# Performance work log

Measured on AMD Instinct MI355X. Metric: run time of the kernel, lower is better.

The kernel has to match this reference:

```python
import jax, jax.numpy as jnp
import numpy as np
from jax import lax

# Model hyperparameters (from module source: D_state=2, Expand=1; mamba-ssm defaults)
B_, C_, H_, W_ = 16, 128, 96, 96
D_MODEL = C_
D_INNER = 1 * D_MODEL          # expand = 1
D_STATE = 2
DT_RANK = (D_MODEL + 15) // 16  # ceil(d_model/16) = 8
D_CONV = 4
OUT_C = 128
LN_EPS = 1e-5


def setup_inputs() -> dict:
    key = jax.random.key(0)
    ks = jax.random.split(key, 10)
    s = 0.02
    x = jax.random.normal(ks[0], (B_, C_, H_, W_), dtype=jnp.float32)
    in_proj_w = jax.random.normal(ks[1], (2 * D_INNER, D_MODEL), dtype=jnp.float32) * s
    conv_w = jax.random.normal(ks[2], (D_INNER, 1, D_CONV), dtype=jnp.float32) * s
    conv_b = jnp.zeros((D_INNER,), dtype=jnp.float32)
    x_proj_w = jax.random.normal(ks[3], (DT_RANK + 2 * D_STATE, D_INNER), dtype=jnp.float32) * s
    dt_proj_w = jax.random.normal(ks[4], (D_INNER, DT_RANK), dtype=jnp.float32) * s
    # softplus^{-1}(0.01) so initial dt ~ 0.01 (standard mamba init)
    dt_proj_b = jnp.full((D_INNER,), float(np.log(np.expm1(0.01))), dtype=jnp.float32)
    A_log = jnp.log(jnp.broadcast_to(jnp.arange(1, D_STATE + 1, dtype=jnp.float32), (D_INNER, D_STATE)))
    D_param = jnp.ones((D_INNER,), dtype=jnp.float32)
    out_proj_w = jax.random.normal(ks[5], (OUT_C, D_INNER), dtype=jnp.float32) * s
    ln_gamma = jnp.ones((OUT_C,), dtype=jnp.float32)
    ln_beta = jnp.zeros((OUT_C,), dtype=jnp.float32)
    return {
        "x": x, "in_proj_w": in_proj_w, "conv_w": conv_w, "conv_b": conv_b,
        "x_proj_w": x_proj_w, "dt_proj_w": dt_proj_w, "dt_proj_b": dt_proj_b,
        "A_log": A_log, "D_param": D_param, "out_proj_w": out_proj_w,
        "ln_gamma": ln_gamma, "ln_beta": ln_beta,
    }


def _ssm_cha(x, in_proj_w, conv_w, conv_b, x_proj_w, dt_proj_w, dt_proj_b,
             A_log, D_param, out_proj_w, ln_gamma, ln_beta):
    b, c, h, w = x.shape
    L = h * w
    tokens = x.transpose(0, 2, 3, 1).reshape(b, L, c)  # [b, L, d_model]

    # in_proj -> (x_in, z)
    xz = jnp.einsum("bld,ed->ble", tokens, in_proj_w)  # [b, L, 2*d_inner]
    x_in, z = jnp.split(xz, 2, axis=-1)

    # causal depthwise conv1d over L, then SiLU
    xc = x_in.transpose(0, 2, 1)  # [b, d_inner, L]
    xc = lax.conv_general_dilated(
        xc, conv_w, window_strides=(1,), padding=[(D_CONV - 1, 0)],
        dimension_numbers=("NCH", "OIH", "NCH"), feature_group_count=D_INNER,
    ) + conv_b[None, :, None]
    x_in = jax.nn.silu(xc).transpose(0, 2, 1)  # [b, L, d_inner]

    # x_proj -> (dt, B, C)
    x_dbl = jnp.einsum("bld,ed->ble", x_in, x_proj_w)
    dt = x_dbl[..., :DT_RANK]
    Bc = x_dbl[..., DT_RANK:DT_RANK + D_STATE]         # [b, L, n]
    Cc = x_dbl[..., DT_RANK + D_STATE:]                # [b, L, n]
    dt = jax.nn.softplus(jnp.einsum("blr,dr->bld", dt, dt_proj_w) + dt_proj_b)

    # selective scan (diagonal A) via associative scan over L
    A = -jnp.exp(A_log)                                # [d_inner, n]
    dA = jnp.exp(dt[..., None] * A)                    # [b, L, d_inner, n]
    dBx = dt[..., None] * Bc[:, :, None, :] * x_in[..., None]

    def combine(e1, e2):
        a1, b1 = e1
        a2, b2 = e2
        return a1 * a2, a2 * b1 + b2

    _, hstate = lax.associative_scan(combine, (dA, dBx), axis=1)  # [b, L, d, n]
    y = jnp.sum(hstate * Cc[:, :, None, :], axis=-1) + D_param * x_in  # [b, L, d]

    y = y * jax.nn.silu(z)
    out = jnp.einsum("bld,od->blo", y, out_proj_w)     # [b, L, out_c]

    # LayerNorm over out_c
    mu = jnp.mean(out, axis=-1, keepdims=True)
    var = jnp.mean(jnp.square(out - mu), axis=-1, keepdims=True)
    out = (out - mu) * lax.rsqrt(var + LN_EPS) * ln_gamma + ln_beta

    return out.reshape(b, h, w, OUT_C).transpose(0, 3, 1, 2)


def reference(x, in_proj_w, conv_w, conv_b, x_proj_w, dt_proj_w, dt_proj_b,
              A_log, D_param, out_proj_w, ln_gamma, ln_beta):
    return _ssm_cha(x, in_proj_w, conv_w, conv_b, x_proj_w, dt_proj_w, dt_proj_b,
                    A_log, D_param, out_proj_w, ln_gamma, ln_beta)
```

## Files before the change

### kernel.cpp

```cpp
#include <hip/hip_runtime.h>
#include <hip/hip_bf16.h>

#define B_N 16
#define L_N 9216
#define LT64 144

typedef __attribute__((ext_vector_type(8))) short short8;
typedef __attribute__((ext_vector_type(4))) float floatx4;

__device__ __forceinline__ float bfu(unsigned short u) {
  return __uint_as_float(((unsigned int)u) << 16);
}
__device__ __forceinline__ unsigned short fbf(float f) {
  __hip_bfloat16 h = __float2bfloat16(f);
  return *(unsigned short*)&h;
}

__global__ __launch_bounds__(256) void k_prep(const float* __restrict__ w1,
                                              const float* __restrict__ w2,
                                              __hip_bfloat16* __restrict__ w1bt,
                                              __hip_bfloat16* __restrict__ w2bt) {
  int i = blockIdx.x * 256 + threadIdx.x;
  if (i < 256 * 128) w1bt[i] = __float2bfloat16(w1[i]);
  if (i < 128 * 128) w2bt[i] = __float2bfloat16(w2[i]);
}

__global__ __launch_bounds__(256) void k_inproj_conv(
    const float* __restrict__ x, const __hip_bfloat16* __restrict__ w1bt,
    const float* __restrict__ cw, const float* __restrict__ cb,
    const float* __restrict__ xpw,
    __hip_bfloat16* __restrict__ xinb, __hip_bfloat16* __restrict__ zb,
    float* __restrict__ xdblT) {
  __shared__ __align__(16) char smem1[16384];
  __shared__ __align__(16) char smem2[34816];
  __hip_bfloat16* xs = (__hip_bfloat16*)smem1;
  float (*red)[12][64] = (float(*)[12][64])smem1;
  unsigned short (*st)[73] = (unsigned short(*)[73])smem2;
  float (*cvs)[68] = (float(*)[68])smem2;

  int blk = blockIdx.x, b = blk / LT64, lt = blk % LT64, l0 = lt * 64;
  int t = threadIdx.x;

  const float* xb = x + (size_t)b * 128 * L_N + (l0 - 8);
#pragma unroll
  for (int i = 0; i < 9; ++i) {
    int idx = t + i * 256;
    int c = idx / 18, q = idx % 18;
    float4 v;
    if (lt == 0 && q < 2) { v.x = 0.f; v.y = 0.f; v.z = 0.f; v.w = 0.f; }
    else v = *(const float4*)(xb + (size_t)c * L_N + q * 4);
    st[c][q * 4 + 0] = fbf(v.x); st[c][q * 4 + 1] = fbf(v.y);
    st[c][q * 4 + 2] = fbf(v.z); st[c][q * 4 + 3] = fbf(v.w);
  }

  int lane = t & 63, wv = t >> 6;
  int col = lane & 15, quad = lane >> 4;
  int e0 = wv * 64;
  short8 afr[4][4];
  const __hip_bfloat16* wb = w1bt + (size_t)(e0 + col) * 128 + quad * 8;
#pragma unroll
  for (int mi = 0; mi < 4; ++mi)
#pragma unroll
    for (int ks = 0; ks < 4; ++ks)
      afr[mi][ks] = *(const short8*)(wb + mi * 16 * 128 + ks * 32);

  __syncthreads();

#pragma unroll
  for (int p = 0; p < 4; ++p) {
    int gi = t + p * 256;
    int l = gi >> 4, ch = gi & 15;
    short8 cc;
#pragma unroll
    for (int j = 0; j < 8; ++j) cc[j] = (short)st[ch * 8 + j][8 + l];
    *(short8*)&xs[l * 128 + ((ch ^ (l & 7)) * 8)] = cc;
  }

  floatx4 vzero = {0.f, 0.f, 0.f, 0.f};
  floatx4 acc[4][4];
#pragma unroll
  for (int mi = 0; mi < 4; ++mi)
#pragma unroll
    for (int ni = 0; ni < 4; ++ni) acc[mi][ni] = vzero;
  __syncthreads();

#pragma unroll
  for (int ks = 0; ks < 4; ++ks) {
    short8 bfr[4];
#pragma unroll
    for (int ni = 0; ni < 4; ++ni) {
      int row = ni * 16 + col;
      bfr[ni] = *(const short8*)&xs[row * 128 + (((ks * 4 + quad) ^ (row & 7)) * 8)];
    }
#pragma unroll
    for (int mi = 0; mi < 4; ++mi)
#pragma unroll
      for (int ni = 0; ni < 4; ++ni)
        acc[mi][ni] = __builtin_amdgcn_mfma_f32_16x16x32_bf16(afr[mi][ks], bfr[ni], acc[mi][ni], 0, 0, 0);
  }

  float s0 = 0.f, s1 = 0.f, s2 = 0.f;
  if (t < 128 && lt > 0) {
    const __hip_bfloat16* wr = w1bt + (size_t)t * 128;
#pragma unroll
    for (int c8 = 0; c8 < 16; ++c8) {
      short8 wc = *(const short8*)(wr + c8 * 8);
#pragma unroll
      for (int e = 0; e < 8; ++e) {
        int c = c8 * 8 + e;
        float wf = bfu((unsigned short)wc[e]);
        s0 += wf * bfu(st[c][5]);
        s1 += wf * bfu(st[c][6]);
        s2 += wf * bfu(st[c][7]);
      }
    }
  }
  if (wv >= 2) {
    __hip_bfloat16* zbase = zb + ((size_t)b * 128 + (e0 - 128)) * L_N + l0;
#pragma unroll
    for (int mi = 0; mi < 4; ++mi)
#pragma unroll
      for (int r = 0; r < 4; ++r) {
        int dr = mi * 16 + quad * 4 + r;
#pragma unroll
        for (int ni = 0; ni < 4; ++ni)
          zbase[(size_t)dr * L_N + ni * 16 + col] = __float2bfloat16(acc[mi][ni][r]);
      }
  }
  __syncthreads();

  if (t < 128) { cvs[t][0] = s0; cvs[t][1] = s1; cvs[t][2] = s2; }
  if (wv < 2) {
#pragma unroll
    for (int mi = 0; mi < 4; ++mi)
#pragma unroll
      for (int r = 0; r < 4; ++r) {
        int d = e0 + mi * 16 + quad * 4 + r;
#pragma unroll
        for (int ni = 0; ni < 4; ++ni) cvs[d][3 + ni * 16 + col] = acc[mi][ni][r];
      }
  }
  __syncthreads();

  float part[12];
#pragma unroll
  for (int m = 0; m < 12; ++m) part[m] = 0.f;
  for (int dd = 0; dd < 32; ++dd) {
    int d = wv * 32 + dd;
    float v = cb[d] + cw[d * 4 + 0] * cvs[d][lane] + cw[d * 4 + 1] * cvs[d][lane + 1]
                    + cw[d * 4 + 2] * cvs[d][lane + 2] + cw[d * 4 + 3] * cvs[d][lane + 3];
    v = v / (1.f + __expf(-v));
    xinb[((size_t)b * 128 + d) * L_N + l0 + lane] = __float2bfloat16(v);
#pragma unroll
    for (int m = 0; m < 12; ++m) part[m] += xpw[m * 128 + d] * v;
  }
#pragma unroll
  for (int m = 0; m < 12; ++m) red[wv][m][lane] = part[m];
  __syncthreads();
  for (int idx = t; idx < 12 * 64; idx += 256) {
    int m = idx >> 6, l = idx & 63;
    float s = red[0][m][l] + red[1][m][l] + red[2][m][l] + red[3][m][l];
    xdblT[((size_t)b * 12 + m) * L_N + l0 + l] = s;
  }
}

__global__ __launch_bounds__(256) void k_scan(
    const float* __restrict__ xdblT, const float* __restrict__ dtw,
    const float* __restrict__ dtb, const float* __restrict__ alog,
    const float* __restrict__ dpar,
    const __hip_bfloat16* __restrict__ xinb, const __hip_bfloat16* __restrict__ zb,
    __hip_bfloat16* __restrict__ yb) {
  __shared__ float agg[4][4];
  __shared__ float carry[2];
  int blk = blockIdx.x, b = blk >> 7, d = blk & 127;
  int t = threadIdx.x, lane = t & 63, wv = t >> 6;
  float A0 = -__expf(alog[2 * d]), A1 = -__expf(alog[2 * d + 1]);
  float Dv = dpar[d], dtbv = dtb[d];
  float w[8];
#pragma unroll
  for (int i = 0; i < 8; ++i) w[i] = dtw[d * 8 + i];
  if (t == 0) { carry[0] = 0.f; carry[1] = 0.f; }
  __syncthreads();
  const float* xdT = xdblT + (size_t)b * 12 * L_N;
  const unsigned short* xi = (const unsigned short*)xinb + ((size_t)b * 128 + d) * L_N;
  const unsigned short* zr = (const unsigned short*)zb + ((size_t)b * 128 + d) * L_N;
  unsigned short* yo = (unsigned short*)yb + ((size_t)b * 128 + d) * L_N;
  for (int it = 0; it < 9; ++it) {
    int lb = it * 1024 + t * 4;
    float4 q[12];
#pragma unroll
    for (int m = 0; m < 12; ++m) q[m] = *(const float4*)(xdT + (size_t)m * L_N + lb);
    ushort4 xu = *(const ushort4*)(xi + lb);
    ushort4 zu = *(const ushort4*)(zr + lb);
    float xv[4] = {bfu(xu.x), bfu(xu.y), bfu(xu.z), bfu(xu.w)};
    float zv[4] = {bfu(zu.x), bfu(zu.y), bfu(zu.z), bfu(zu.w)};
    float A0p[4], X0p[4], A1p[4], X1p[4];
#pragma unroll
    for (int j = 0; j < 4; ++j) {
      float dtp = dtbv;
#pragma unroll
      for (int m = 0; m < 8; ++m) dtp += w[m] * ((const float*)&q[m])[j];
      float dt = (dtp > 15.f) ? dtp : __logf(1.f + __expf(dtp));
      float a0 = __expf(dt * A0), a1 = __expf(dt * A1);
      float dtx = dt * xv[j];
      float x0 = dtx * ((const float*)&q[8])[j];
      float x1 = dtx * ((const float*)&q[9])[j];
      if (j == 0) { A0p[0] = a0; X0p[0] = x0; A1p[0] = a1; X1p[0] = x1; }
      else {
        A0p[j] = a0 * A0p[j - 1]; X0p[j] = a0 * X0p[j - 1] + x0;
        A1p[j] = a1 * A1p[j - 1]; X1p[j] = a1 * X1p[j - 1] + x1;
      }
    }
    float wA0 = A0p[3], wX0 = X0p[3], wA1 = A1p[3], wX1 = X1p[3];
#pragma unroll
    for (int off = 1; off < 64; off <<= 1) {
      float pA0 = __shfl_up(wA0, off, 64), pX0 = __shfl_up(wX0, off, 64);
      float pA1 = __shfl_up(wA1, off, 64), pX1 = __shfl_up(wX1, off, 64);
      if (lane >= off) {
        wX0 += wA0 * pX0; wA0 *= pA0;
        wX1 += wA1 * pX1; wA1 *= pA1;
      }
    }
    if (lane == 63) { agg[wv][0] = wA0; agg[wv][1] = wX0; agg[wv][2] = wA1; agg[wv][3] = wX1; }
    float eA0 = __shfl_up(wA0, 1, 64), eX0 = __shfl_up(wX0, 1, 64);
    float eA1 = __shfl_up(wA1, 1, 64), eX1 = __shfl_up(wX1, 1, 64);
    if (lane == 0) { eA0 = 1.f; eX0 = 0.f; eA1 = 1.f; eX1 = 0.f; }
    __syncthreads();
    float h0 = carry[0], h1 = carry[1];
    for (int jw = 0; jw < wv; ++jw) {
      h0 = agg[jw][0] * h0 + agg[jw][1];
      h1 = agg[jw][2] * h1 + agg[jw][3];
    }
    h0 = eA0 * h0 + eX0;
    h1 = eA1 * h1 + eX1;
    __syncthreads();
    if (t == 255) { carry[0] = A0p[3] * h0 + X0p[3]; carry[1] = A1p[3] * h1 + X1p[3]; }
    ushort4 yu;
    unsigned short* yp = (unsigned short*)&yu;
#pragma unroll
    for (int j = 0; j < 4; ++j) {
      float hh0 = A0p[j] * h0 + X0p[j];
      float hh1 = A1p[j] * h1 + X1p[j];
      float y = hh0 * ((const float*)&q[10])[j] + hh1 * ((const float*)&q[11])[j] + Dv * xv[j];
      y *= zv[j] / (1.f + __expf(-zv[j]));
      yp[j] = fbf(y);
    }
    *(ushort4*)(yo + lb) = yu;
  }
}

__global__ __launch_bounds__(256) void k_outln(
    const __hip_bfloat16* __restrict__ yb, const __hip_bfloat16* __restrict__ w2bt,
    const float* __restrict__ gam, const float* __restrict__ bet,
    float* __restrict__ out) {
  __shared__ unsigned short st[128][68];
  __shared__ __hip_bfloat16 yts[64 * 128];
  __shared__ float red_s[4][64], red_q[4][64];
  __shared__ float gs[128], bs[128];
  int blk = blockIdx.x, b = blk / LT64, lt = blk % LT64, l0 = lt * 64;
  int t = threadIdx.x;
  if (t < 128) { gs[t] = gam[t]; bs[t] = bet[t]; }
  const unsigned short* ybb = (const unsigned short*)yb + (size_t)b * 128 * L_N + l0;
#pragma unroll
  for (int i = 0; i < 8; ++i) {
    int idx = t + i * 256;
    int dd = idx >> 4, l4 = (idx & 15) * 4;
    ushort4 v = *(const ushort4*)(ybb + (size_t)dd * L_N + l4);
    *(ushort4*)&st[dd][l4] = v;
  }
  __syncthreads();
#pragma unroll
  for (int p = 0; p < 4; ++p) {
    int gi = t + p * 256;
    int l = gi & 63, ch = gi >> 6;
    short8 c;
#pragma unroll
    for (int j = 0; j < 8; ++j) c[j] = (short)st[ch * 8 + j][l];
    *(short8*)&yts[l * 128 + ((ch ^ (l & 7)) * 8)] = c;
  }
  int lane = t & 63, wv = t >> 6;
  int col = lane & 15, quad = lane >> 4;
  int o0 = wv * 32;
  short8 afr[2][4];
#pragma unroll
  for (int mi = 0; mi < 2; ++mi)
#pragma unroll
    for (int ks = 0; ks < 4; ++ks)
      afr[mi][ks] = *(const short8*)(w2bt + (size_t)(o0 + mi * 16 + col) * 128 + ks * 32 + quad * 8);
  floatx4 vzero = {0.f, 0.f, 0.f, 0.f};
  floatx4 acc[2][4];
#pragma unroll
  for (int mi = 0; mi < 2; ++mi)
#pragma unroll
    for (int ni = 0; ni < 4; ++ni) acc[mi][ni] = vzero;
  __syncthreads();
#pragma unroll
  for (int ks = 0; ks < 4; ++ks) {
    short8 bfr[4];
#pragma unroll
    for (int ni = 0; ni < 4; ++ni) {
      int row = ni * 16 + col;
      bfr[ni] = *(const short8*)&yts[row * 128 + (((ks * 4 + quad) ^ (row & 7)) * 8)];
    }
#pragma unroll
    for (int mi = 0; mi < 2; ++mi)
#pragma unroll
      for (int ni = 0; ni < 4; ++ni)
        acc[mi][ni] = __builtin_amdgcn_mfma_f32_16x16x32_bf16(afr[mi][ks], bfr[ni], acc[mi][ni], 0, 0, 0);
  }
  float s[4], q[4];
#pragma unroll
  for (int ni = 0; ni < 4; ++ni) {
    float ss = 0.f, qq = 0.f;
#pragma unroll
    for (int mi = 0; mi < 2; ++mi)
#pragma unroll
      for (int r = 0; r < 4; ++r) {
        float v = acc[mi][ni][r];
        ss += v; qq += v * v;
      }
    ss += __shfl_xor(ss, 16, 64); ss += __shfl_xor(ss, 32, 64);
    qq += __shfl_xor(qq, 16, 64); qq += __shfl_xor(qq, 32, 64);
    s[ni] = ss; q[ni] = qq;
  }
  if (quad == 0) {
#pragma unroll
    for (int ni = 0; ni < 4; ++ni) {
      red_s[wv][ni * 16 + col] = s[ni];
      red_q[wv][ni * 16 + col] = q[ni];
    }
  }
  __syncthreads();
  float mu[4], rstd[4];
#pragma unroll
  for (int ni = 0; ni < 4; ++ni) {
    int li = ni * 16 + col;
    float ts = red_s[0][li] + red_s[1][li] + red_s[2][li] + red_s[3][li];
    float tq = red_q[0][li] + red_q[1][li] + red_q[2][li] + red_q[3][li];
    float m = ts * (1.f / 128.f);
    float var = tq * (1.f / 128.f) - m * m;
    mu[ni] = m;
    rstd[ni] = rsqrtf(var + 1e-5f);
  }
  float* ob = out + (size_t)b * 128 * L_N;
#pragma unroll
  for (int mi = 0; mi < 2; ++mi)
#pragma unroll
    for (int r = 0; r < 4; ++r) {
      int o = o0 + mi * 16 + quad * 4 + r;
      float g = gs[o], bb = bs[o];
#pragma unroll
      for (int ni = 0; ni < 4; ++ni)
        ob[(size_t)o * L_N + l0 + ni * 16 + col] = (acc[mi][ni][r] - mu[ni]) * rstd[ni] * g + bb;
    }
}

extern "C" void kernel_launch(void* const* d_in, const int* in_sizes, int n_in,
                              void* d_out, int out_size, void* d_ws, size_t ws_size,
                              hipStream_t stream) {
  const float* x    = (const float*)d_in[0];
  const float* w1   = (const float*)d_in[1];
  const float* cw   = (const float*)d_in[2];
  const float* cb   = (const float*)d_in[3];
  const float* xpw  = (const float*)d_in[4];
  const float* dtw  = (const float*)d_in[5];
  const float* dtb  = (const float*)d_in[6];
  const float* alog = (const float*)d_in[7];
  const float* dpar = (const float*)d_in[8];
  const float* w2   = (const float*)d_in[9];
  const float* gam  = (const float*)d_in[10];
  const float* bet  = (const float*)d_in[11];
  float* out = (float*)d_out;

  float* ws = (float*)d_ws;
  const size_t NBL = (size_t)B_N * 128 * L_N;
  float* xdblT = ws;
  __hip_bfloat16* xinb = (__hip_bfloat16*)(ws + (size_t)B_N * 12 * L_N);
  __hip_bfloat16* zb   = xinb + NBL;
  __hip_bfloat16* yb   = zb + NBL;
  __hip_bfloat16* w1bt = yb + NBL;
  __hip_bfloat16* w2bt = w1bt + 256 * 128;

  k_prep<<<128, 256, 0, stream>>>(w1, w2, w1bt, w2bt);
  k_inproj_conv<<<B_N * LT64, 256, 0, stream>>>(x, w1bt, cw, cb, xpw, xinb, zb, xdblT);
  k_scan<<<B_N * 128, 256, 0, stream>>>(xdblT, dtw, dtb, alog, dpar, xinb, zb, yb);
  k_outln<<<B_N * LT64, 256, 0, stream>>>(yb, w2bt, gam, bet, out);
}
```

Baseline: 321.6 us.

## Halve in-proj/conv shared memory by direct swizzled staging and two-pass conv

The x tile is now converted and written straight into the swizzled bf16 GEMM operand layout, with only the 3-column causal halo kept in a small separate buffer. This removes the intermediate transposed staging array and its extra barrier and transpose pass. The conv/SiLU/x_proj stage is split into two 64-channel passes so the conv buffer holds half the channels, roughly halving LDS per block to allow more resident blocks. The cost is an extra pair of barriers and scattered 2-byte LDS writes with possible bank conflicts during staging.

```diff
diff --git a/kernel.cpp b/kernel.cpp
--- a/kernel.cpp
+++ b/kernel.cpp
@@ -32,49 +32,46 @@
     __hip_bfloat16* __restrict__ xinb, __hip_bfloat16* __restrict__ zb,
     float* __restrict__ xdblT) {
   __shared__ __align__(16) char smem1[16384];
-  __shared__ __align__(16) char smem2[34816];
-  __hip_bfloat16* xs = (__hip_bfloat16*)smem1;
+  __shared__ __align__(16) char smem2[17408];
+  unsigned short* xs = (unsigned short*)smem1;
   float (*red)[12][64] = (float(*)[12][64])smem1;
-  unsigned short (*st)[73] = (unsigned short(*)[73])smem2;
+  unsigned short (*halo)[128] = (unsigned short(*)[128])smem2;
   float (*cvs)[68] = (float(*)[68])smem2;
 
   int blk = blockIdx.x, b = blk / LT64, lt = blk % LT64, l0 = lt * 64;
   int t = threadIdx.x;
+  int lane = t & 63, wv = t >> 6;
+  int col = lane & 15, quad = lane >> 4;
+  int e0 = wv * 64;
 
   const float* xb = x + (size_t)b * 128 * L_N + (l0 - 8);
 #pragma unroll
   for (int i = 0; i < 9; ++i) {
     int idx = t + i * 256;
-    int c = idx / 18, q = idx % 18;
+    int c = idx & 127, q = idx >> 7;
+    if (q == 0) continue;
     float4 v;
     if (lt == 0 && q < 2) { v.x = 0.f; v.y = 0.f; v.z = 0.f; v.w = 0.f; }
     else v = *(const float4*)(xb + (size_t)c * L_N + q * 4);
-    st[c][q * 4 + 0] = fbf(v.x); st[c][q * 4 + 1] = fbf(v.y);
-    st[c][q * 4 + 2] = fbf(v.z); st[c][q * 4 + 3] = fbf(v.w);
-  }
-
-  int lane = t & 63, wv = t >> 6;
-  int col = lane & 15, quad = lane >> 4;
-  int e0 = wv * 64;
+    if (q < 2) {
+      halo[4][c] = fbf(v.x); halo[5][c] = fbf(v.y);
+      halo[6][c] = fbf(v.z); halo[7][c] = fbf(v.w);
+    } else {
+      int l = q * 4 - 8;
+      xs[(l + 0) * 128 + ((((c >> 3) ^ ((l + 0) & 7)) << 3) | (c & 7))] = fbf(v.x);
+      xs[(l + 1) * 128 + ((((c >> 3) ^ ((l + 1) & 7)) << 3) | (c & 7))] = fbf(v.y);
+      xs[(l + 2) * 128 + ((((c >> 3) ^ ((l + 2) & 7)) << 3) | (c & 7))] = fbf(v.z);
+      xs[(l + 3) * 128 + ((((c >> 3) ^ ((l + 3) & 7)) << 3) | (c & 7))] = fbf(v.w);
+    }
+  }
+
   short8 afr[4][4];
-  const __hip_bfloat16* wb = w1bt + (size_t)(e0 + col) * 128 + quad * 8;
+  const __hip_bfloat16* wbp = w1bt + (size_t)(e0 + col) * 128 + quad * 8;
 #pragma unroll
   for (int mi = 0; mi < 4; ++mi)
 #pragma unroll
     for (int ks = 0; ks < 4; ++ks)
-      afr[mi][ks] = *(const short8*)(wb + mi * 16 * 128 + ks * 32);
-
-  __syncthreads();
-
-#pragma unroll
-  for (int p = 0; p < 4; ++p) {
-    int gi = t + p * 256;
-    int l = gi >> 4, ch = gi & 15;
-    short8 cc;
-#pragma unroll
-    for (int j = 0; j < 8; ++j) cc[j] = (short)st[ch * 8 + j][8 + l];
-    *(short8*)&xs[l * 128 + ((ch ^ (l & 7)) * 8)] = cc;
-  }
+      afr[mi][ks] = *(const short8*)(wbp + mi * 16 * 128 + ks * 32);
 
   floatx4 vzero = {0.f, 0.f, 0.f, 0.f};
   floatx4 acc[4][4];
@@ -90,7 +87,7 @@
 #pragma unroll
     for (int ni = 0; ni < 4; ++ni) {
       int row = ni * 16 + col;
-      bfr[ni] = *(const short8*)&xs[row * 128 + (((ks * 4 + quad) ^ (row & 7)) * 8)];
+      bfr[ni] = *(const short8*)&xs[row * 128 + (((ks * 4 + quad) ^ (row & 7)) << 3)];
     }
 #pragma unroll
     for (int mi = 0; mi < 4; ++mi)
@@ -105,16 +102,19 @@
 #pragma unroll
     for (int c8 = 0; c8 < 16; ++c8) {
       short8 wc = *(const short8*)(wr + c8 * 8);
+      short8 h5 = *(const short8*)&halo[5][c8 * 8];
+      short8 h6 = *(const short8*)&halo[6][c8 * 8];
+      short8 h7 = *(const short8*)&halo[7][c8 * 8];
 #pragma unroll
       for (int e = 0; e < 8; ++e) {
-        int c = c8 * 8 + e;
         float wf = bfu((unsigned short)wc[e]);
-        s0 += wf * bfu(st[c][5]);
-        s1 += wf * bfu(st[c][6]);
-        s2 += wf * bfu(st[c][7]);
-      }
-    }
-  }
+        s0 += wf * bfu((unsigned short)h5[e]);
+        s1 += wf * bfu((unsigned short)h6[e]);
+        s2 += wf * bfu((unsigned short)h7[e]);
+      }
+    }
+  }
+
   if (wv >= 2) {
     __hip_bfloat16* zbase = zb + ((size_t)b * 128 + (e0 - 128)) * L_N + l0;
 #pragma unroll
@@ -129,13 +129,13 @@
   }
   __syncthreads();
 
-  if (t < 128) { cvs[t][0] = s0; cvs[t][1] = s1; cvs[t][2] = s2; }
-  if (wv < 2) {
+  if (t < 64) { cvs[t][0] = s0; cvs[t][1] = s1; cvs[t][2] = s2; }
+  if (wv == 0) {
 #pragma unroll
     for (int mi = 0; mi < 4; ++mi)
 #pragma unroll
       for (int r = 0; r < 4; ++r) {
-        int d = e0 + mi * 16 + quad * 4 + r;
+        int d = mi * 16 + quad * 4 + r;
 #pragma unroll
         for (int ni = 0; ni < 4; ++ni) cvs[d][3 + ni * 16 + col] = acc[mi][ni][r];
       }
@@ -145,10 +145,34 @@
   float part[12];
 #pragma unroll
   for (int m = 0; m < 12; ++m) part[m] = 0.f;
-  for (int dd = 0; dd < 32; ++dd) {
-    int d = wv * 32 + dd;
+  for (int dd = 0; dd < 16; ++dd) {
+    int d = wv * 16 + dd;
     float v = cb[d] + cw[d * 4 + 0] * cvs[d][lane] + cw[d * 4 + 1] * cvs[d][lane + 1]
                     + cw[d * 4 + 2] * cvs[d][lane + 2] + cw[d * 4 + 3] * cvs[d][lane + 3];
+    v = v / (1.f + __expf(-v));
+    xinb[((size_t)b * 128 + d) * L_N + l0 + lane] = __float2bfloat16(v);
+#pragma unroll
+    for (int m = 0; m < 12; ++m) part[m] += xpw[m * 128 + d] * v;
+  }
+  __syncthreads();
+
+  if (t >= 64 && t < 128) { cvs[t - 64][0] = s0; cvs[t - 64][1] = s1; cvs[t - 64][2] = s2; }
+  if (wv == 1) {
+#pragma unroll
+    for (int mi = 0; mi < 4; ++mi)
+#pragma unroll
+      for (int r = 0; r < 4; ++r) {
+        int rr = mi * 16 + quad * 4 + r;
+#pragma unroll
+        for (int ni = 0; ni < 4; ++ni) cvs[rr][3 + ni * 16 + col] = acc[mi][ni][r];
+      }
+  }
+  __syncthreads();
+
+  for (int dd = 0; dd < 16; ++dd) {
+    int rr = wv * 16 + dd, d = 64 + rr;
+    float v = cb[d] + cw[d * 4 + 0] * cvs[rr][lane] + cw[d * 4 + 1] * cvs[rr][lane + 1]
+                    + cw[d * 4 + 2] * cvs[rr][lane + 2] + cw[d * 4 + 3] * cvs[rr][lane + 3];
     v = v / (1.f + __expf(-v));
     xinb[((size_t)b * 128 + d) * L_N + l0 + lane] = __float2bfloat16(v);
 #pragma unroll
```

New measurement: 309.8 us. 3.7% less time.

## Precompute conv halo in separate kernel and widen in-proj blocks to 512 threads

Applied to the files above, without the earlier changes.

Moves the causal-conv halo projection (three boundary tokens per tile) into a new prep kernel that also converts the weights, writing the results to a workspace buffer. The in-proj/conv kernel now runs 512 threads with 8 waves, each handling 32 output rows. Its input is converted straight into the swizzled LDS layout, skipping the staging transpose, and A fragments are software-prefetched one k-step ahead. The aim is to cut LDS staging and register pressure and to raise occupancy, at the cost of an extra global round trip for the halo values and an extra barrier.

```diff
diff --git a/kernel.cpp b/kernel.cpp
--- a/kernel.cpp
+++ b/kernel.cpp
@@ -16,109 +16,116 @@
   return *(unsigned short*)&h;
 }
 
-__global__ __launch_bounds__(256) void k_prep(const float* __restrict__ w1,
-                                              const float* __restrict__ w2,
-                                              __hip_bfloat16* __restrict__ w1bt,
-                                              __hip_bfloat16* __restrict__ w2bt) {
-  int i = blockIdx.x * 256 + threadIdx.x;
-  if (i < 256 * 128) w1bt[i] = __float2bfloat16(w1[i]);
-  if (i < 128 * 128) w2bt[i] = __float2bfloat16(w2[i]);
-}
-
-__global__ __launch_bounds__(256) void k_inproj_conv(
+__global__ __launch_bounds__(256) void k_bnd(const float* __restrict__ x,
+                                             const float* __restrict__ w1,
+                                             const float* __restrict__ w2,
+                                             __hip_bfloat16* __restrict__ w1bt,
+                                             __hip_bfloat16* __restrict__ w2bt,
+                                             float* __restrict__ bndbuf) {
+  int blk = blockIdx.x, t = threadIdx.x;
+  int gi = blk * 256 + t;
+  if (gi < 256 * 128) w1bt[gi] = __float2bfloat16(w1[gi]);
+  else if (gi < 256 * 128 + 128 * 128) {
+    int j = gi - 256 * 128;
+    w2bt[j] = __float2bfloat16(w2[j]);
+  }
+  int b = blk / LT64, lt = blk % LT64;
+  if (lt == 0) return;
+  int l0 = lt * 64;
+  __shared__ float xst[128][4];
+  if (t < 128) {
+    float4 v = *(const float4*)(x + ((size_t)b * 128 + t) * L_N + l0 - 4);
+    xst[t][0] = v.x; xst[t][1] = v.y; xst[t][2] = v.z; xst[t][3] = v.w;
+  }
+  __syncthreads();
+  if (t < 128) {
+    const float4* wr = (const float4*)(w1 + (size_t)t * 128);
+    float s0 = 0.f, s1 = 0.f, s2 = 0.f;
+#pragma unroll
+    for (int c4 = 0; c4 < 32; ++c4) {
+      float4 w4 = wr[c4];
+      int c = c4 * 4;
+      s0 += w4.x * xst[c][1] + w4.y * xst[c + 1][1] + w4.z * xst[c + 2][1] + w4.w * xst[c + 3][1];
+      s1 += w4.x * xst[c][2] + w4.y * xst[c + 1][2] + w4.z * xst[c + 2][2] + w4.w * xst[c + 3][2];
+      s2 += w4.x * xst[c][3] + w4.y * xst[c + 1][3] + w4.z * xst[c + 2][3] + w4.w * xst[c + 3][3];
+    }
+    float* o = bndbuf + ((size_t)(b * LT64 + lt) * 128 + t) * 3;
+    o[0] = s0; o[1] = s1; o[2] = s2;
+  }
+}
+
+__global__ __launch_bounds__(512, 4) void k_inproj_conv(
     const float* __restrict__ x, const __hip_bfloat16* __restrict__ w1bt,
     const float* __restrict__ cw, const float* __restrict__ cb,
-    const float* __restrict__ xpw,
+    const float* __restrict__ xpw, const float* __restrict__ bndbuf,
     __hip_bfloat16* __restrict__ xinb, __hip_bfloat16* __restrict__ zb,
     float* __restrict__ xdblT) {
   __shared__ __align__(16) char smem1[16384];
   __shared__ __align__(16) char smem2[34816];
-  __hip_bfloat16* xs = (__hip_bfloat16*)smem1;
-  float (*red)[12][64] = (float(*)[12][64])smem1;
-  unsigned short (*st)[73] = (unsigned short(*)[73])smem2;
+  unsigned short* xs = (unsigned short*)smem1;
   float (*cvs)[68] = (float(*)[68])smem2;
+  float (*red)[12][64] = (float(*)[12][64])smem2;
 
   int blk = blockIdx.x, b = blk / LT64, lt = blk % LT64, l0 = lt * 64;
   int t = threadIdx.x;
-
-  const float* xb = x + (size_t)b * 128 * L_N + (l0 - 8);
-#pragma unroll
-  for (int i = 0; i < 9; ++i) {
-    int idx = t + i * 256;
-    int c = idx / 18, q = idx % 18;
-    float4 v;
-    if (lt == 0 && q < 2) { v.x = 0.f; v.y = 0.f; v.z = 0.f; v.w = 0.f; }
-    else v = *(const float4*)(xb + (size_t)c * L_N + q * 4);
-    st[c][q * 4 + 0] = fbf(v.x); st[c][q * 4 + 1] = fbf(v.y);
-    st[c][q * 4 + 2] = fbf(v.z); st[c][q * 4 + 3] = fbf(v.w);
-  }
-
   int lane = t & 63, wv = t >> 6;
   int col = lane & 15, quad = lane >> 4;
-  int e0 = wv * 64;
-  short8 afr[4][4];
-  const __hip_bfloat16* wb = w1bt + (size_t)(e0 + col) * 128 + quad * 8;
-#pragma unroll
-  for (int mi = 0; mi < 4; ++mi)
-#pragma unroll
-    for (int ks = 0; ks < 4; ++ks)
-      afr[mi][ks] = *(const short8*)(wb + mi * 16 * 128 + ks * 32);
-
-  __syncthreads();
-
-#pragma unroll
-  for (int p = 0; p < 4; ++p) {
-    int gi = t + p * 256;
-    int l = gi >> 4, ch = gi & 15;
-    short8 cc;
-#pragma unroll
-    for (int j = 0; j < 8; ++j) cc[j] = (short)st[ch * 8 + j][8 + l];
-    *(short8*)&xs[l * 128 + ((ch ^ (l & 7)) * 8)] = cc;
-  }
-
+
+  const float* xb = x + (size_t)b * 128 * L_N + l0;
+#pragma unroll
+  for (int i = 0; i < 4; ++i) {
+    int idx = t + i * 512;
+    int c = idx & 127, q = idx >> 7;
+    float4 v = *(const float4*)(xb + (size_t)c * L_N + q * 4);
+    int ch = c >> 3, ce = c & 7;
+#pragma unroll
+    for (int j = 0; j < 4; ++j) {
+      int l = q * 4 + j;
+      xs[l * 128 + (((ch ^ (l & 7)) << 3) | ce)] = fbf(((const float*)&v)[j]);
+    }
+  }
+  if (t < 384) {
+    float bv = (lt > 0) ? bndbuf[(size_t)(b * LT64 + lt) * 128 * 3 + t] : 0.f;
+    cvs[t / 3][t % 3] = bv;
+  }
+
+  int e0 = wv * 32;
+  const __hip_bfloat16* wbp = w1bt + (size_t)(e0 + col) * 128 + quad * 8;
   floatx4 vzero = {0.f, 0.f, 0.f, 0.f};
-  floatx4 acc[4][4];
-#pragma unroll
-  for (int mi = 0; mi < 4; ++mi)
+  floatx4 acc[2][4];
+#pragma unroll
+  for (int mi = 0; mi < 2; ++mi)
 #pragma unroll
     for (int ni = 0; ni < 4; ++ni) acc[mi][ni] = vzero;
+  short8 a0 = *(const short8*)(wbp);
+  short8 a1 = *(const short8*)(wbp + 16 * 128);
   __syncthreads();
 
 #pragma unroll
   for (int ks = 0; ks < 4; ++ks) {
+    short8 n0, n1;
+    if (ks < 3) {
+      n0 = *(const short8*)(wbp + (ks + 1) * 32);
+      n1 = *(const short8*)(wbp + 16 * 128 + (ks + 1) * 32);
+    }
     short8 bfr[4];
 #pragma unroll
     for (int ni = 0; ni < 4; ++ni) {
       int row = ni * 16 + col;
-      bfr[ni] = *(const short8*)&xs[row * 128 + (((ks * 4 + quad) ^ (row & 7)) * 8)];
-    }
-#pragma unroll
-    for (int mi = 0; mi < 4; ++mi)
-#pragma unroll
-      for (int ni = 0; ni < 4; ++ni)
-        acc[mi][ni] = __builtin_amdgcn_mfma_f32_16x16x32_bf16(afr[mi][ks], bfr[ni], acc[mi][ni], 0, 0, 0);
-  }
-
-  float s0 = 0.f, s1 = 0.f, s2 = 0.f;
-  if (t < 128 && lt > 0) {
-    const __hip_bfloat16* wr = w1bt + (size_t)t * 128;
-#pragma unroll
-    for (int c8 = 0; c8 < 16; ++c8) {
-      short8 wc = *(const short8*)(wr + c8 * 8);
-#pragma unroll
-      for (int e = 0; e < 8; ++e) {
-        int c = c8 * 8 + e;
-        float wf = bfu((unsigned short)wc[e]);
-        s0 += wf * bfu(st[c][5]);
-        s1 += wf * bfu(st[c][6]);
-        s2 += wf * bfu(st[c][7]);
-      }
-    }
-  }
-  if (wv >= 2) {
+      bfr[ni] = *(const short8*)&xs[row * 128 + (((ks * 4 + quad) ^ (row & 7)) << 3)];
+    }
+#pragma unroll
+    for (int ni = 0; ni < 4; ++ni) {
+      acc[0][ni] = __builtin_amdgcn_mfma_f32_16x16x32_bf16(a0, bfr[ni], acc[0][ni], 0, 0, 0);
+      acc[1][ni] = __builtin_amdgcn_mfma_f32_16x16x32_bf16(a1, bfr[ni], acc[1][ni], 0, 0, 0);
+    }
+    a0 = n0; a1 = n1;
+  }
+
+  if (wv >= 4) {
     __hip_bfloat16* zbase = zb + ((size_t)b * 128 + (e0 - 128)) * L_N + l0;
 #pragma unroll
-    for (int mi = 0; mi < 4; ++mi)
+    for (int mi = 0; mi < 2; ++mi)
 #pragma unroll
       for (int r = 0; r < 4; ++r) {
         int dr = mi * 16 + quad * 4 + r;
@@ -126,13 +133,9 @@
         for (int ni = 0; ni < 4; ++ni)
           zbase[(size_t)dr * L_N + ni * 16 + col] = __float2bfloat16(acc[mi][ni][r]);
       }
-  }
-  __syncthreads();
-
-  if (t < 128) { cvs[t][0] = s0; cvs[t][1] = s1; cvs[t][2] = s2; }
-  if (wv < 2) {
-#pragma unroll
-    for (int mi = 0; mi < 4; ++mi)
+  } else {
+#pragma unroll
+    for (int mi = 0; mi < 2; ++mi)
 #pragma unroll
       for (int r = 0; r < 4; ++r) {
         int d = e0 + mi * 16 + quad * 4 + r;
@@ -145,8 +148,8 @@
   float part[12];
 #pragma unroll
   for (int m = 0; m < 12; ++m) part[m] = 0.f;
-  for (int dd = 0; dd < 32; ++dd) {
-    int d = wv * 32 + dd;
+  for (int dd = 0; dd < 16; ++dd) {
+    int d = wv * 16 + dd;
     float v = cb[d] + cw[d * 4 + 0] * cvs[d][lane] + cw[d * 4 + 1] * cvs[d][lane + 1]
                     + cw[d * 4 + 2] * cvs[d][lane + 2] + cw[d * 4 + 3] * cvs[d][lane + 3];
     v = v / (1.f + __expf(-v));
@@ -154,12 +157,15 @@
 #pragma unroll
     for (int m = 0; m < 12; ++m) part[m] += xpw[m * 128 + d] * v;
   }
+  __syncthreads();
 #pragma unroll
   for (int m = 0; m < 12; ++m) red[wv][m][lane] = part[m];
   __syncthreads();
-  for (int idx = t; idx < 12 * 64; idx += 256) {
+  for (int idx = t; idx < 12 * 64; idx += 512) {
     int m = idx >> 6, l = idx & 63;
-    float s = red[0][m][l] + red[1][m][l] + red[2][m][l] + red[3][m][l];
+    float s = 0.f;
+#pragma unroll
+    for (int w8 = 0; w8 < 8; ++w8) s += red[w8][m][l];
     xdblT[((size_t)b * 12 + m) * L_N + l0 + l] = s;
   }
 }
@@ -380,9 +386,10 @@
   __hip_bfloat16* yb   = zb + NBL;
   __hip_bfloat16* w1bt = yb + NBL;
   __hip_bfloat16* w2bt = w1bt + 256 * 128;
-
-  k_prep<<<128, 256, 0, stream>>>(w1, w2, w1bt, w2bt);
-  k_inproj_conv<<<B_N * LT64, 256, 0, stream>>>(x, w1bt, cw, cb, xpw, xinb, zb, xdblT);
+  float* bndbuf = (float*)(w2bt + 128 * 128);
+
+  k_bnd<<<B_N * LT64, 256, 0, stream>>>(x, w1, w2, w1bt, w2bt, bndbuf);
+  k_inproj_conv<<<B_N * LT64, 512, 0, stream>>>(x, w1bt, cw, cb, xpw, bndbuf, xinb, zb, xdblT);
   k_scan<<<B_N * 128, 256, 0, stream>>>(xdblT, dtw, dtb, alog, dpar, xinb, zb, yb);
   k_outln<<<B_N * LT64, 256, 0, stream>>>(yb, w2bt, gam, bet, out);
 }
```

Result: faster. 309.9 us (-3.7%).
